# Optimization experiments

Hardware: AMD Instinct MI355X
Metric: run time of the kernel (lower is better)

## Reference

```python
import jax, jax.numpy as jnp
import numpy as np

K = 4          # neighbors
R = 2          # step_ratio
O = 64         # output_size


def setup_inputs() -> dict:
    key = jax.random.key(0)
    ks = jax.random.split(key, 7)
    B, C, N = 16, 128, 2048
    x = jax.random.normal(ks[0], (B, C, N), jnp.float32)
    # 1x1 conv weights stored as [out, in]; bias [out]
    w1 = jax.random.normal(ks[1], (O, 2 * C), jnp.float32) * (1.0 / np.sqrt(2 * C))
    b1 = jax.random.normal(ks[2], (O,), jnp.float32) * 0.01
    w2 = jax.random.normal(ks[3], (O * R, 2 * C + O), jnp.float32) * (1.0 / np.sqrt(2 * C + O))
    b2 = jax.random.normal(ks[4], (O * R,), jnp.float32) * 0.01
    w3 = jax.random.normal(ks[5], (O, O), jnp.float32) * (1.0 / np.sqrt(O))
    b3 = jax.random.normal(ks[6], (O,), jnp.float32) * 0.01
    return {"x": x, "w1": w1, "b1": b1, "w2": w2, "b2": b2, "w3": w3, "b3": b3}


def _knn_idx(x, k):
    # x: [B, C, N]; returns indices of k nearest neighbors (incl. self) [B, N, k]
    inner = -2.0 * jnp.einsum('bcn,bcm->bnm', x, x)           # [B, N, N]
    xx = jnp.sum(x * x, axis=1)                                # [B, N]
    pd = -xx[:, :, None] - inner - xx[:, None, :]              # negative sq dist
    return jax.lax.top_k(pd, k)[1]                             # [B, N, k]


def _graph_feature(x, k):
    # minus_center=False variant used by EF_expansion
    idx = _knn_idx(x, k)                                       # [B, N, k]
    xt = jnp.transpose(x, (0, 2, 1))                           # [B, N, C]
    feat = jax.vmap(lambda xb, ib: xb[ib])(xt, idx)            # [B, N, k, C]
    center = jnp.broadcast_to(xt[:, :, None, :], feat.shape)   # [B, N, k, C]
    f = jnp.concatenate([center, feat], axis=3)                # [B, N, k, 2C]
    return jnp.transpose(f, (0, 3, 1, 2))                      # [B, 2C, N, k]


def _conv1x1(w, b, x):
    # x: [B, Cin, H, W] -> [B, Cout, H, W]
    return jnp.einsum('oc,bchw->bohw', w, x) + b[None, :, None, None]


def reference(x, w1, b1, w2, b2, w3, b3):
    B, C, N = x.shape
    ief = jnp.transpose(_graph_feature(x, K), (0, 1, 3, 2))    # [B, 2C, k, N]
    e1 = _conv1x1(w1, b1, ief)                                 # [B, O, k, N]
    e = jax.nn.relu(jnp.concatenate([e1, ief], axis=1))        # [B, O+2C, k, N]
    e2 = jax.nn.relu(_conv1x1(w2, b2, e))                      # [B, O*R, k, N]
    # [B,O*R,k,N] -> [B,k,N,O*R] -> [B,k,N*R,O] -> [B,O,k,N*R]
    e2 = jnp.transpose(e2, (0, 2, 3, 1)).reshape(B, K, N * R, O)
    e2 = jnp.transpose(e2, (0, 3, 1, 2))
    e3 = _conv1x1(w3, b3, e2)                                  # [B, O, k, N*R]
    return jnp.max(e3, axis=2)                                 # [B, O, N*R]
```

## Files before the change

### kernel.cpp

```cpp
#include <hip/hip_runtime.h>
#include <cstdint>
#include <cstddef>

#define B_  16
#define C_  128
#define N_  2048
#define K_  4
#define O_  64
#define C2_ 256
#define ED_ 320
#define NM_ 4096
#define AGC 384

typedef float  f32x4  __attribute__((ext_vector_type(4)));
typedef short  s16x8  __attribute__((ext_vector_type(8)));
typedef __bf16 bf16x4 __attribute__((ext_vector_type(4)));
typedef __bf16 bf16x8 __attribute__((ext_vector_type(8)));
typedef unsigned short u16;
typedef unsigned int   u32;
typedef unsigned int   u32x4 __attribute__((ext_vector_type(4)));

__device__ __forceinline__ u32 umin32(u32 a, u32 b) { return a < b ? a : b; }
__device__ __forceinline__ u32 umax32(u32 a, u32 b) { return a > b ? a : b; }
__device__ __forceinline__ float bf2f(u16 h) { return __builtin_bit_cast(float, (u32)h << 16); }

__device__ __forceinline__ s16x8 ldw_bf16(const float* __restrict__ p) {
  float4 a = *(const float4*)p;
  float4 c = *(const float4*)(p + 4);
  bf16x8 r;
  r[0] = (__bf16)a.x; r[1] = (__bf16)a.y; r[2] = (__bf16)a.z; r[3] = (__bf16)a.w;
  r[4] = (__bf16)c.x; r[5] = (__bf16)c.y; r[6] = (__bf16)c.z; r[7] = (__bf16)c.w;
  return __builtin_bit_cast(s16x8, r);
}

__device__ __forceinline__ u32 relu2(u32 u) {
  u32 s = u & 0x80008000u;
  u32 m = s - (s >> 15);
  return u & ~(m | s);
}
__device__ __forceinline__ s16x8 relu8(s16x8 v) {
  u32x4 u = __builtin_bit_cast(u32x4, v);
  u[0] = relu2(u[0]); u[1] = relu2(u[1]);
  u[2] = relu2(u[2]); u[3] = relu2(u[3]);
  return __builtin_bit_cast(s16x8, u);
}

__device__ __forceinline__ void glds16(const void* g, void* l) {
  __builtin_amdgcn_global_load_lds(
      (const __attribute__((address_space(1))) u32*)g,
      (__attribute__((address_space(3))) u32*)l, 16, 0, 0);
}

__global__ __launch_bounds__(256) void prep_kernel(const float* __restrict__ x,
                                                   const float* __restrict__ w1,
                                                   const float* __restrict__ w2,
                                                   const float* __restrict__ w3,
                                                   float* __restrict__ xT32,
                                                   u16* __restrict__ xh,
                                                   float* __restrict__ xx,
                                                   u16* __restrict__ wh,
                                                   u16* __restrict__ wg) {
  const int t = threadIdx.x;
  if (blockIdx.y == B_) {
    const int gid = blockIdx.x * 256 + t;
    for (int i = gid; i < 15360; i += 8192) {
      const float* src; u16* dst;
      if (i < 4096)       { src = w1 + (size_t)i * 4;            dst = wh + (size_t)i * 4; }
      else if (i < 14336) { src = w2 + (size_t)(i - 4096) * 4;   dst = wh + 16384 + (size_t)(i - 4096) * 4; }
      else                { src = w3 + (size_t)(i - 14336) * 4;  dst = wh + 57344 + (size_t)(i - 14336) * 4; }
      float4 v = *(const float4*)src;
      ushort4 h;
      h.x = __builtin_bit_cast(u16, (__bf16)v.x);
      h.y = __builtin_bit_cast(u16, (__bf16)v.y);
      h.z = __builtin_bit_cast(u16, (__bf16)v.z);
      h.w = __builtin_bit_cast(u16, (__bf16)v.w);
      *(ushort4*)dst = h;
    }
    if (wg) {
      for (int i = gid; i < 12288; i += 8192) {
        int r = i >> 5;
        int c4 = (i & 31) * 4;
        const float* src;
        if (r < 64)       src = w1 + (size_t)r * C2_ + c4;
        else if (r < 128) src = w1 + (size_t)(r - 64) * C2_ + 128 + c4;
        else if (r < 256) src = w2 + (size_t)(r - 128) * ED_ + 64 + c4;
        else              src = w2 + (size_t)(r - 256) * ED_ + 192 + c4;
        float4 v = *(const float4*)src;
        ushort4 h;
        h.x = __builtin_bit_cast(u16, (__bf16)v.x);
        h.y = __builtin_bit_cast(u16, (__bf16)v.y);
        h.z = __builtin_bit_cast(u16, (__bf16)v.z);
        h.w = __builtin_bit_cast(u16, (__bf16)v.w);
        *(ushort4*)&wg[(size_t)r * 128 + c4] = h;
      }
    }
    return;
  }

  __shared__ __align__(16) float sx[C_][65];
  const int b = blockIdx.y, n0 = blockIdx.x * 64;
  const float* xb = x + (size_t)b * C_ * N_;
  for (int u = t; u < C_ * 16; u += 256) {
    int c = u >> 4, f4 = u & 15;
    float4 v = *(const float4*)&xb[(size_t)c * N_ + n0 + f4 * 4];
    sx[c][f4 * 4 + 0] = v.x; sx[c][f4 * 4 + 1] = v.y;
    sx[c][f4 * 4 + 2] = v.z; sx[c][f4 * 4 + 3] = v.w;
  }
  __syncthreads();
  if (t < 64) {
    float s = 0.f;
    for (int c = 0; c < C_; ++c) { float v = sx[c][t]; s = fmaf(v, v, s); }
    xx[b * N_ + n0 + t] = s;
  }
  for (int u = t; u < 64 * 16; u += 256) {
    int n = u >> 4, cb = u & 15;
    float vv[8]; s16x8 hv;
#pragma unroll
    for (int j = 0; j < 8; ++j) {
      float v = sx[cb * 8 + j][n];
      vv[j] = v;
      hv[j] = (short)__builtin_bit_cast(u16, (__bf16)v);
    }
    size_t ro = ((size_t)b * N_ + n0 + n) * C_;
    *(float4*)&xT32[ro + cb * 8]     = make_float4(vv[0], vv[1], vv[2], vv[3]);
    *(float4*)&xT32[ro + cb * 8 + 4] = make_float4(vv[4], vv[5], vv[6], vv[7]);
    int sc = cb ^ (n & 7);
    *(s16x8*)&xh[ro + sc * 8] = hv;
  }
}

__global__ __launch_bounds__(256) void knn_mfma(const u16* __restrict__ xh,
                                                const float* __restrict__ xx,
                                                int* __restrict__ cand8) {
  __shared__ __align__(16) u32 cd[64 * 85];
  const int b = blockIdx.y, q0 = blockIdx.x * 64;
  const int t = threadIdx.x;
  const int wv = t >> 6, lq = t & 15, lh = (t >> 4) & 3;
  const u16* xhb = xh + (size_t)b * N_ * C_;
  const float* xxb = xx + b * N_;

  s16x8 qf[4][4];
#pragma unroll
  for (int qt = 0; qt < 4; ++qt)
#pragma unroll
    for (int ks = 0; ks < 4; ++ks) {
      int q = q0 + qt * 16 + lq;
      int ch = (ks * 4 + lh) ^ (q & 7);
      qf[qt][ks] = *(const s16x8*)&xhb[(size_t)q * C_ + ch * 8];
    }

  u32 pk[4][5];
#pragma unroll
  for (int qt = 0; qt < 4; ++qt)
#pragma unroll
    for (int s = 0; s < 5; ++s) pk[qt][s] = 0xFFFFFFFFu;

  const int rbase = wv * 16 + lq;
  int choff[4];
#pragma unroll
  for (int ks = 0; ks < 4; ++ks) choff[ks] = ((ks * 4 + lh) ^ (lq & 7)) * 8;

  auto loadf = [&](int step, s16x8* d) {
    const u16* rp = xhb + (size_t)(step * 64 + rbase) * C_;
#pragma unroll
    for (int ks = 0; ks < 4; ++ks) d[ks] = *(const s16x8*)&rp[choff[ks]];
  };
  auto dostep = [&](int step, const s16x8* mf) {
    f32x4 acc[4];
#pragma unroll
    for (int qt = 0; qt < 4; ++qt) acc[qt] = (f32x4){0.f, 0.f, 0.f, 0.f};
#pragma unroll
    for (int ks = 0; ks < 4; ++ks)
#pragma unroll
      for (int qt = 0; qt < 4; ++qt)
        acc[qt] = __builtin_amdgcn_mfma_f32_16x16x32_bf16(mf[ks], qf[qt][ks], acc[qt], 0, 0, 0);
    const int mrow = step * 64 + wv * 16 + lh * 4;
    float4 xm4 = *(const float4*)&xxb[mrow];
    float xma[4] = {xm4.x + 512.f, xm4.y + 512.f, xm4.z + 512.f, xm4.w + 512.f};
#pragma unroll
    for (int r = 0; r < 4; ++r) {
#pragma unroll
      for (int qt = 0; qt < 4; ++qt) {
        float dd = fmaf(acc[qt][r], -2.f, xma[r]);
        u32 u = __builtin_bit_cast(u32, dd);
        u32 v = (u & 0xFFFFF800u) | (u32)(mrow + r);
#pragma unroll
        for (int s5 = 0; s5 < 5; ++s5) {
          u32 lo = umin32(v, pk[qt][s5]);
          v = umax32(v, pk[qt][s5]);
          pk[qt][s5] = lo;
        }
      }
    }
  };

  s16x8 fa[4], fb[4];
  loadf(0, fa);
  loadf(1, fb);
  for (int step = 0; step < 32; step += 2) {
    dostep(step, fa);
    if (step + 2 < 32) loadf(step + 2, fa);
    dostep(step + 1, fb);
    if (step + 3 < 32) loadf(step + 3, fb);
  }

  const int unit = wv * 4 + lh;
#pragma unroll
  for (int qt = 0; qt < 4; ++qt) {
    int ql = qt * 16 + lq;
#pragma unroll
    for (int s = 0; s < 5; ++s) cd[ql * 85 + unit * 5 + s] = pk[qt][s];
  }
  __syncthreads();
  if (t < 64) {
    u32 fd[8];
#pragma unroll
    for (int s = 0; s < 8; ++s) fd[s] = 0xFFFFFFFFu;
    for (int j = 0; j < 80; ++j) {
      u32 v = cd[t * 85 + j];
#pragma unroll
      for (int s = 0; s < 8; ++s) {
        u32 lo = umin32(v, fd[s]);
        v = umax32(v, fd[s]);
        fd[s] = lo;
      }
    }
#pragma unroll
    for (int s = 0; s < 8; ++s)
      cand8[((size_t)b * N_ + q0 + t) * 8 + s] = (int)(fd[s] & 0x7FFu);
  }
}

__global__ __launch_bounds__(256) void rerank_kernel(const float* __restrict__ xT32,
                                                     const float* __restrict__ xx,
                                                     const int* __restrict__ cand8,
                                                     int* __restrict__ knn_out) {
  __shared__ __align__(16) float sq[64][132];
  __shared__ float sd[64][8];
  __shared__ int   si[64][8];
  const int b = blockIdx.y, n0 = blockIdx.x * 64;
  const int t = threadIdx.x;
  const float* xb32 = xT32 + (size_t)b * N_ * C_;
  for (int u = t; u < 64 * 32; u += 256) {
    int n = u >> 5, seg = u & 31;
    *(float4*)&sq[n][seg * 4] = *(const float4*)&xb32[(size_t)(n0 + n) * C_ + seg * 4];
  }
  __syncthreads();
  const int ql = t >> 2, cs = t & 3;
#pragma unroll
  for (int cc = 0; cc < 2; ++cc) {
    int cslot = cs + cc * 4;
    int idx = cand8[((size_t)b * N_ + n0 + ql) * 8 + cslot];
    const float* mr = &xb32[(size_t)idx * C_];
    float a0 = 0.f, a1 = 0.f, a2 = 0.f, a3 = 0.f;
#pragma unroll 8
    for (int i = 0; i < 32; ++i) {
      float4 qv = *(const float4*)&sq[ql][i * 4];
      float4 mv = *(const float4*)&mr[i * 4];
      a0 = fmaf(qv.x, mv.x, a0); a1 = fmaf(qv.y, mv.y, a1);
      a2 = fmaf(qv.z, mv.z, a2); a3 = fmaf(qv.w, mv.w, a3);
    }
    float dot = (a0 + a1) + (a2 + a3);
    sd[ql][cslot] = xx[(size_t)b * N_ + idx] - 2.f * dot;
    si[ql][cslot] = idx;
  }
  __syncthreads();
  if (t < 64) {
    float dloc[8]; int iloc[8];
#pragma unroll
    for (int j = 0; j < 8; ++j) { dloc[j] = sd[t][j]; iloc[j] = si[t][j]; }
    u32 used = 0;
#pragma unroll
    for (int s = 0; s < 4; ++s) {
      float bdv = 1e30f; int bidx = 0x7fffffff; int bj = 0;
#pragma unroll
      for (int j = 0; j < 8; ++j) {
        if (!((used >> j) & 1)) {
          bool bet = (dloc[j] < bdv) || (dloc[j] == bdv && iloc[j] < bidx);
          if (bet) { bdv = dloc[j]; bidx = iloc[j]; bj = j; }
        }
      }
      used |= 1u << bj;
      knn_out[((size_t)b * N_ + n0 + t) * K_ + s] = bidx;
    }
  }
}

__global__ __launch_bounds__(256, 2) void agemm_kernel(
    const u16* __restrict__ xh, const u16* __restrict__ wg,
    const float* __restrict__ b1, const float* __restrict__ b2,
    u16* __restrict__ ag) {
  __shared__ __align__(16) char sm[66560];
  u16* outT = (u16*)(sm + 16384);
  const int b = blockIdx.y, m0 = blockIdx.x * 64;
  const int t = threadIdx.x, lane = t & 63, wv = t >> 6, lq = t & 15, lh = (t >> 4) & 3;
  const u16* xhb = xh + (size_t)b * N_ * C_;

  {
    const char* s = (const char*)(xhb + (size_t)m0 * C_);
#pragma unroll
    for (int c = 0; c < 4; ++c) {
      int off = (wv * 4 + c) * 1024;
      glds16(s + off + lane * 16, sm + off);
    }
  }

  s16x8 af[6][4];
#pragma unroll
  for (int rt = 0; rt < 6; ++rt)
#pragma unroll
    for (int ks = 0; ks < 4; ++ks)
      af[rt][ks] = *(const s16x8*)&wg[(size_t)(wv * 96 + rt * 16 + lq) * 128 + ks * 32 + lh * 8];

  f32x4 acc[6][4];
#pragma unroll
  for (int rt = 0; rt < 6; ++rt)
#pragma unroll
    for (int cg = 0; cg < 4; ++cg) acc[rt][cg] = (f32x4){0.f, 0.f, 0.f, 0.f};

  asm volatile("s_waitcnt vmcnt(0)");
  __syncthreads();

#pragma unroll
  for (int cg = 0; cg < 4; ++cg) {
    s16x8 braw[4], brel[4];
#pragma unroll
    for (int ks = 0; ks < 4; ++ks) {
      int row = cg * 16 + lq;
      braw[ks] = *(const s16x8*)(sm + row * 256 + (((ks * 4 + lh) ^ (lq & 7)) * 16));
      brel[ks] = relu8(braw[ks]);
    }
#pragma unroll
    for (int rt = 0; rt < 6; ++rt) {
      const bool rl = (wv * 96 + rt * 16) >= 128;
#pragma unroll
      for (int ks = 0; ks < 4; ++ks)
        acc[rt][cg] = __builtin_amdgcn_mfma_f32_16x16x32_bf16(
            af[rt][ks], rl ? brel[ks] : braw[ks], acc[rt][cg], 0, 0, 0);
    }
  }

#pragma unroll
  for (int rt = 0; rt < 6; ++rt) {
    const int ch0 = wv * 96 + rt * 16 + lh * 4;
    float bias[4];
#pragma unroll
    for (int r = 0; r < 4; ++r) {
      int c = ch0 + r;
      bias[r] = (c < 64) ? b1[c] : ((c >= 128 && c < 256) ? b2[c - 128] : 0.f);
    }
#pragma unroll
    for (int cg = 0; cg < 4; ++cg) {
      bf16x4 st;
#pragma unroll
      for (int r = 0; r < 4; ++r) st[r] = (__bf16)(acc[rt][cg][r] + bias[r]);
      *(bf16x4*)&outT[(size_t)(cg * 16 + lq) * 392 + ch0] = st;
    }
  }
  __syncthreads();

  {
    const int row = t >> 2, p = t & 3;
#pragma unroll
    for (int k = 0; k < 12; ++k) {
      int seg = k * 4 + p;
      *(u32x4*)&ag[((size_t)b * N_ + m0 + row) * AGC + seg * 8] =
          *(const u32x4*)&outT[(size_t)row * 392 + seg * 8];
    }
  }
}

__global__ __launch_bounds__(256, 3) void fused_ag(
    const u16* __restrict__ ag, const u16* __restrict__ wh,
    const int* __restrict__ knn_idx,
    const float* __restrict__ b3, float* __restrict__ out) {
  __shared__ __align__(16) char fsm[44032];
  u16* e1T = (u16*)fsm;
  u16* s2T = (u16*)(fsm + 9216);
  u16* e2T = (u16*)(fsm + 26624);
  float* oSt = (float*)fsm;

  const int t = threadIdx.x, wv = t >> 6, lq = t & 15, lh = (t >> 4) & 3;
  const int b = blockIdx.y, n0 = blockIdx.x * 16;
  const u16* agb = ag + (size_t)b * N_ * AGC;
  const u16* w2h = wh + 16384;
  const u16* w3h = wh + 57344;

  s16x8 w2f[2][2];
#pragma unroll
  for (int rt = 0; rt < 2; ++rt)
#pragma unroll
    for (int ks = 0; ks < 2; ++ks)
      w2f[rt][ks] = *(const s16x8*)&w2h[(size_t)(wv * 32 + rt * 16 + lq) * ED_ + ks * 32 + lh * 8];
  const s16x8 w3a = *(const s16x8*)&w3h[(size_t)(wv * 16 + lq) * O_ + lh * 8];
  const s16x8 w3b = *(const s16x8*)&w3h[(size_t)(wv * 16 + lq) * O_ + 32 + lh * 8];
  const float4 b3v = *(const float4*)&b3[wv * 16 + lh * 4];

  {
    const int col = t >> 2, p = t & 3;
    const int n = n0 + (col >> 2);
    const int nid = knn_idx[((size_t)b * N_ + n) * K_ + (col & 3)];
    const u16* rc = agb + (size_t)n * AGC;
    const u16* rn = agb + (size_t)nid * AGC;
#pragma unroll
    for (int q = 0; q < 2; ++q) {
      s16x8 va = *(const s16x8*)&rc[p * 16 + q * 8];
      s16x8 vb = *(const s16x8*)&rn[64 + p * 16 + q * 8];
      bf16x8 r;
#pragma unroll
      for (int j = 0; j < 8; ++j)
        r[j] = (__bf16)fmaxf(bf2f((u16)va[j]) + bf2f((u16)vb[j]), 0.f);
      *(bf16x8*)&e1T[(size_t)col * 72 + p * 16 + q * 8] = r;
    }
#pragma unroll
    for (int q = 0; q < 4; ++q) {
      s16x8 va = *(const s16x8*)&rc[128 + p * 32 + q * 8];
      s16x8 vb = *(const s16x8*)&rn[256 + p * 32 + q * 8];
      bf16x8 r;
#pragma unroll
      for (int j = 0; j < 8; ++j)
        r[j] = (__bf16)(bf2f((u16)va[j]) + bf2f((u16)vb[j]));
      *(bf16x8*)&s2T[(size_t)col * 136 + p * 32 + q * 8] = r;
    }
  }
  __syncthreads();

  {
    f32x4 acc[2][4];
#pragma unroll
    for (int rt = 0; rt < 2; ++rt)
#pragma unroll
      for (int cg = 0; cg < 4; ++cg) acc[rt][cg] = (f32x4){0.f, 0.f, 0.f, 0.f};
#pragma unroll
    for (int ks = 0; ks < 2; ++ks)
#pragma unroll
      for (int cg = 0; cg < 4; ++cg) {
        s16x8 bf = *(const s16x8*)&e1T[(size_t)(cg * 16 + lq) * 72 + ks * 32 + lh * 8];
#pragma unroll
        for (int rt = 0; rt < 2; ++rt)
          acc[rt][cg] = __builtin_amdgcn_mfma_f32_16x16x32_bf16(w2f[rt][ks], bf, acc[rt][cg], 0, 0, 0);
      }
#pragma unroll
    for (int rt = 0; rt < 2; ++rt)
#pragma unroll
      for (int cg = 0; cg < 4; ++cg) {
        const int col = cg * 16 + lq;
        const int j0 = wv * 32 + rt * 16 + lh * 4;
        ushort4 sv = *(const ushort4*)&s2T[(size_t)col * 136 + j0];
        bf16x4 st;
        st[0] = (__bf16)fmaxf(acc[rt][cg][0] + bf2f(sv.x), 0.f);
        st[1] = (__bf16)fmaxf(acc[rt][cg][1] + bf2f(sv.y), 0.f);
        st[2] = (__bf16)fmaxf(acc[rt][cg][2] + bf2f(sv.z), 0.f);
        st[3] = (__bf16)fmaxf(acc[rt][cg][3] + bf2f(sv.w), 0.f);
        *(bf16x4*)&e2T[(size_t)col * 136 + j0] = st;
      }
  }
  __syncthreads();

  {
#pragma unroll
    for (int cg = 0; cg < 8; ++cg) {
      int col = cg * 16 + lq;
      int nl = col >> 3, rr = (col >> 2) & 1, kk = col & 3;
      int row = nl * 4 + kk;
      s16x8 f1 = *(const s16x8*)&e2T[(size_t)row * 136 + rr * 64 + lh * 8];
      s16x8 f2 = *(const s16x8*)&e2T[(size_t)row * 136 + rr * 64 + 32 + lh * 8];
      f32x4 acc = {0.f, 0.f, 0.f, 0.f};
      acc = __builtin_amdgcn_mfma_f32_16x16x32_bf16(w3a, f1, acc, 0, 0, 0);
      acc = __builtin_amdgcn_mfma_f32_16x16x32_bf16(w3b, f2, acc, 0, 0, 0);
      float vv[4];
#pragma unroll
      for (int r = 0; r < 4; ++r) {
        float v = acc[r];
        v = fmaxf(v, __shfl_xor(v, 1));
        v = fmaxf(v, __shfl_xor(v, 2));
        vv[r] = v;
      }
      if ((lq & 3) == 0) {
        int mloc = col >> 2;
        int o = wv * 16 + lh * 4;
        const float b3a[4] = {b3v.x, b3v.y, b3v.z, b3v.w};
#pragma unroll
        for (int r = 0; r < 4; ++r) oSt[(size_t)(o + r) * 36 + mloc] = vv[r] + b3a[r];
      }
    }
  }
  __syncthreads();

#pragma unroll
  for (int io = 0; io < 2; ++io) {
    int u = t + io * 256;
    int o = u >> 3, seg = u & 7;
    *(float4*)&out[((size_t)b * O_ + o) * NM_ + n0 * 2 + seg * 4] =
        *(const float4*)&oSt[(size_t)o * 36 + seg * 4];
  }
}

__global__ __launch_bounds__(256) void xx_kernel(const float* __restrict__ x,
                                                 float* __restrict__ xx) {
  int g = blockIdx.x * 256 + threadIdx.x;
  int b = g >> 11;
  int n = g & (N_ - 1);
  const float* xp = x + (size_t)b * C_ * N_ + n;
  float s = 0.f;
#pragma unroll 8
  for (int c = 0; c < C_; ++c) { float v = xp[(size_t)c * N_]; s += v * v; }
  xx[g] = s;
}

__global__ __launch_bounds__(256) void knn_kernel(const float* __restrict__ x,
                                                  const float* __restrict__ xx,
                                                  int* __restrict__ knn_out) {
  __shared__ __align__(16) float qT[C_ * 64];
  __shared__ __align__(16) float mT[C_ * 64];
  const int b = blockIdx.y;
  const int q0 = blockIdx.x * 64;
  const int t = threadIdx.x;
  const float* xb = x + (size_t)b * C_ * N_;
  const float* xxb = xx + b * N_;
  for (int i = t; i < C_ * 64; i += 256) {
    int c = i >> 6, q = i & 63;
    qT[i] = xb[(size_t)c * N_ + q0 + q];
  }
  const int tq = t & 15;
  const int tm = t >> 4;
  float bd[4][4]; int bi[4][4];
#pragma unroll
  for (int a = 0; a < 4; ++a)
#pragma unroll
    for (int s = 0; s < 4; ++s) { bd[a][s] = 1e30f; bi[a][s] = 0; }
  for (int m0 = 0; m0 < N_; m0 += 64) {
    __syncthreads();
    for (int i = t; i < C_ * 64; i += 256) {
      int c = i >> 6, m = i & 63;
      mT[i] = xb[(size_t)c * N_ + m0 + m];
    }
    __syncthreads();
    float acc[4][4];
#pragma unroll
    for (int a = 0; a < 4; ++a)
#pragma unroll
      for (int j = 0; j < 4; ++j) acc[a][j] = 0.f;
#pragma unroll 4
    for (int c = 0; c < C_; ++c) {
      float4 qv = *(const float4*)&qT[c * 64 + tq * 4];
      float4 mv = *(const float4*)&mT[c * 64 + tm * 4];
      float qa[4] = {qv.x, qv.y, qv.z, qv.w};
      float ma[4] = {mv.x, mv.y, mv.z, mv.w};
#pragma unroll
      for (int a = 0; a < 4; ++a)
#pragma unroll
        for (int j = 0; j < 4; ++j) acc[a][j] += qa[a] * ma[j];
    }
#pragma unroll
    for (int j = 0; j < 4; ++j) {
      float xm = xxb[m0 + tm * 4 + j];
      int id = m0 + tm * 4 + j;
#pragma unroll
      for (int a = 0; a < 4; ++a) {
        float d = xm - 2.f * acc[a][j];
        if (d < bd[a][3]) {
          bd[a][3] = d; bi[a][3] = id;
#pragma unroll
          for (int s = 3; s > 0; --s)
            if (bd[a][s] < bd[a][s - 1]) {
              float td = bd[a][s]; bd[a][s] = bd[a][s - 1]; bd[a][s - 1] = td;
              int ti = bi[a][s]; bi[a][s] = bi[a][s - 1]; bi[a][s - 1] = ti;
            }
        }
      }
    }
  }
  __syncthreads();
  float* cd = qT;
  int* ci = (int*)mT;
#pragma unroll
  for (int a = 0; a < 4; ++a) {
    int q = tq * 4 + a;
#pragma unroll
    for (int s = 0; s < 4; ++s) {
      cd[q * 64 + tm * 4 + s] = bd[a][s];
      ci[q * 64 + tm * 4 + s] = bi[a][s];
    }
  }
  __syncthreads();
  if (t < 64) {
    float fd[4]; int fi[4];
#pragma unroll
    for (int s = 0; s < 4; ++s) { fd[s] = 1e30f; fi[s] = 0; }
    for (int j = 0; j < 64; ++j) {
      float d = cd[t * 64 + j];
      int id = ci[t * 64 + j];
      if (d < fd[3]) {
        fd[3] = d; fi[3] = id;
#pragma unroll
        for (int s = 3; s > 0; --s)
          if (fd[s] < fd[s - 1]) {
            float td = fd[s]; fd[s] = fd[s - 1]; fd[s - 1] = td;
            int ti = fi[s]; fi[s] = fi[s - 1]; fi[s - 1] = ti;
          }
      }
    }
#pragma unroll
    for (int s = 0; s < 4; ++s)
      knn_out[(b * N_ + q0 + t) * K_ + s] = fi[s];
  }
}

__global__ __launch_bounds__(256, 5) void fused_fb(
    const float* __restrict__ x, const int* __restrict__ knn_idx,
    const float* __restrict__ w1, const float* __restrict__ b1,
    const float* __restrict__ w2, const float* __restrict__ b2,
    const float* __restrict__ w3, const float* __restrict__ b3,
    float* __restrict__ out) {
  __shared__ __align__(16) char fsm[30976];
  __bf16 (*cT)[136]  = (__bf16(*)[136])(fsm);
  __bf16 (*e1T)[72]  = (__bf16(*)[72])(fsm + 4352);
  float  (*oSt)[36]  = (float(*)[36])(fsm + 4352);
  __bf16 (*nT)[136]  = (__bf16(*)[136])(fsm + 13568);
  __bf16 (*e2T)[136] = (__bf16(*)[136])(fsm + 13568);

  const int b  = blockIdx.y;
  const int n0 = blockIdx.x * 16;
  const int t  = threadIdx.x;
  const float* xb = x + (size_t)b * C_ * N_;

  {
    const int stn = t >> 4, stc = t & 15;
    const int kbase = (b * N_ + n0) * K_;
    const float* srcc = xb + (size_t)(stc * 8) * N_ + n0 + stn;
    bf16x8 raw;
#pragma unroll
    for (int j = 0; j < 8; ++j) raw[j] = (__bf16)srcc[(size_t)j * N_];
    *(bf16x8*)&cT[stn][stc * 8] = raw;
#pragma unroll
    for (int it = 0; it < 4; ++it) {
      int col = stn + 16 * it;
      int nid = knn_idx[kbase + col];
      const float* src = xb + (size_t)(stc * 8) * N_ + nid;
      bf16x8 rw;
#pragma unroll
      for (int j = 0; j < 8; ++j) rw[j] = (__bf16)src[(size_t)j * N_];
      *(bf16x8*)&nT[col][stc * 8] = rw;
    }
  }
  __syncthreads();

  const int lq = t & 15;
  const int lh = (t >> 4) & 3;
  const int wv = t >> 6;

  {
    const float* w1r = w1 + (size_t)(wv * 16 + lq) * C2_;
    f32x4 acc[4];
#pragma unroll
    for (int cg = 0; cg < 4; ++cg) acc[cg] = (f32x4){0.f, 0.f, 0.f, 0.f};
#pragma unroll
    for (int ks = 0; ks < 8; ++ks) {
      s16x8 a = ldw_bf16(w1r + ks * 32 + lh * 8);
#pragma unroll
      for (int cg = 0; cg < 4; ++cg) {
        const __bf16* bp = (ks < 4)
            ? &cT[cg * 4 + (lq >> 2)][ks * 32 + lh * 8]
            : &nT[cg * 16 + lq][(ks - 4) * 32 + lh * 8];
        acc[cg] = __builtin_amdgcn_mfma_f32_16x16x32_bf16(
            a, *(const s16x8*)bp, acc[cg], 0, 0, 0);
      }
    }
#pragma unroll
    for (int cg = 0; cg < 4; ++cg) {
      bf16x4 st;
#pragma unroll
      for (int r = 0; r < 4; ++r) {
        float v = acc[cg][r] + b1[wv * 16 + lh * 4 + r];
        st[r] = (__bf16)fmaxf(v, 0.f);
      }
      *(bf16x4*)&e1T[cg * 16 + lq][wv * 16 + lh * 4] = st;
    }
  }
  __syncthreads();

  f32x4 acc2[2][4];
  {
    const float* w2r0 = w2 + (size_t)(wv * 32 + lq) * ED_;
    const float* w2r1 = w2r0 + (size_t)16 * ED_;
#pragma unroll
    for (int ro = 0; ro < 2; ++ro)
#pragma unroll
      for (int cg = 0; cg < 4; ++cg) acc2[ro][cg] = (f32x4){0.f, 0.f, 0.f, 0.f};
#pragma unroll
    for (int ks = 0; ks < 10; ++ks) {
      s16x8 a0 = ldw_bf16(w2r0 + ks * 32 + lh * 8);
      s16x8 a1 = ldw_bf16(w2r1 + ks * 32 + lh * 8);
#pragma unroll
      for (int cg = 0; cg < 4; ++cg) {
        s16x8 bf;
        if (ks < 2)      bf = *(const s16x8*)&e1T[cg * 16 + lq][ks * 32 + lh * 8];
        else if (ks < 6) bf = relu8(*(const s16x8*)&cT[cg * 4 + (lq >> 2)][(ks - 2) * 32 + lh * 8]);
        else             bf = relu8(*(const s16x8*)&nT[cg * 16 + lq][(ks - 6) * 32 + lh * 8]);
        acc2[0][cg] = __builtin_amdgcn_mfma_f32_16x16x32_bf16(a0, bf, acc2[0][cg], 0, 0, 0);
        acc2[1][cg] = __builtin_amdgcn_mfma_f32_16x16x32_bf16(a1, bf, acc2[1][cg], 0, 0, 0);
      }
    }
  }
  __syncthreads();
  {
#pragma unroll
    for (int ro = 0; ro < 2; ++ro)
#pragma unroll
      for (int cg = 0; cg < 4; ++cg) {
        bf16x4 st;
#pragma unroll
        for (int r = 0; r < 4; ++r) {
          float v = acc2[ro][cg][r] + b2[wv * 32 + ro * 16 + lh * 4 + r];
          st[r] = (__bf16)fmaxf(v, 0.f);
        }
        *(bf16x4*)&e2T[cg * 16 + lq][wv * 32 + ro * 16 + lh * 4] = st;
      }
  }
  __syncthreads();

  {
    const float* w3r = w3 + (size_t)(wv * 16 + lq) * O_;
    s16x8 a0 = ldw_bf16(w3r + lh * 8);
    s16x8 a1 = ldw_bf16(w3r + 32 + lh * 8);
#pragma unroll
    for (int cg = 0; cg < 8; ++cg) {
      int col = cg * 16 + lq;
      int nl = col >> 3, rr = (col >> 2) & 1, kk = col & 3;
      const __bf16* base = &e2T[nl * 4 + kk][rr * 64];
      f32x4 acc = {0.f, 0.f, 0.f, 0.f};
      acc = __builtin_amdgcn_mfma_f32_16x16x32_bf16(a0, *(const s16x8*)(base + lh * 8),      acc, 0, 0, 0);
      acc = __builtin_amdgcn_mfma_f32_16x16x32_bf16(a1, *(const s16x8*)(base + 32 + lh * 8), acc, 0, 0, 0);
      float vv[4];
#pragma unroll
      for (int r = 0; r < 4; ++r) {
        float v = acc[r];
        v = fmaxf(v, __shfl_xor(v, 1));
        v = fmaxf(v, __shfl_xor(v, 2));
        vv[r] = v;
      }
      if ((lq & 3) == 0) {
        int mloc = col >> 2;
        int o = wv * 16 + lh * 4;
#pragma unroll
        for (int r = 0; r < 4; ++r) oSt[o + r][mloc] = vv[r] + b3[o + r];
      }
    }
  }
  __syncthreads();

#pragma unroll
  for (int it = 0; it < 2; ++it) {
    int u = t + it * 256;
    int o = u >> 3, seg = u & 7;
    *(float4*)&out[((size_t)b * O_ + o) * NM_ + n0 * 2 + seg * 4] =
        *(const float4*)&oSt[o][seg * 4];
  }
}

extern "C" void kernel_launch(void* const* d_in, const int* in_sizes, int n_in,
                              void* d_out, int out_size, void* d_ws, size_t ws_size,
                              hipStream_t stream) {
  const float* x  = (const float*)d_in[0];
  const float* w1 = (const float*)d_in[1];
  const float* b1 = (const float*)d_in[2];
  const float* w2 = (const float*)d_in[3];
  const float* b2 = (const float*)d_in[4];
  const float* w3 = (const float*)d_in[5];
  const float* b3 = (const float*)d_in[6];
  float* out = (float*)d_out;

  const size_t AGB      = (size_t)B_ * N_ * AGC * 2;
  const size_t off_c8N  = (size_t)B_ * N_ * C_ * 4;
  const size_t off_xhN  = AGB;
  const size_t off_xxN  = off_xhN + (size_t)B_ * N_ * C_ * 2;
  const size_t off_knnN = off_xxN + (size_t)B_ * N_ * 4;
  const size_t off_whN  = off_knnN + (size_t)B_ * N_ * K_ * 4;
  const size_t off_wgN  = off_whN + (size_t)61440 * 2;
  const size_t NEED_NEW = off_wgN + (size_t)AGC * 128 * 2;

  if (ws_size >= NEED_NEW) {
    u16*   agp  = (u16*)d_ws;
    float* xT32 = (float*)d_ws;
    int*   c8   = (int*)((char*)d_ws + off_c8N);
    u16*   xhp  = (u16*)((char*)d_ws + off_xhN);
    float* xx   = (float*)((char*)d_ws + off_xxN);
    int*   knn  = (int*)((char*)d_ws + off_knnN);
    u16*   whp  = (u16*)((char*)d_ws + off_whN);
    u16*   wgp  = (u16*)((char*)d_ws + off_wgN);

    hipLaunchKernelGGL(prep_kernel, dim3(N_ / 64, B_ + 1), dim3(256), 0, stream,
                       x, w1, w2, w3, xT32, xhp, xx, whp, wgp);
    hipLaunchKernelGGL(knn_mfma, dim3(N_ / 64, B_), dim3(256), 0, stream, xhp, xx, c8);
    hipLaunchKernelGGL(rerank_kernel, dim3(N_ / 64, B_), dim3(256), 0, stream, xT32, xx, c8, knn);
    hipLaunchKernelGGL(agemm_kernel, dim3(N_ / 64, B_), dim3(256), 0, stream,
                       xhp, wgp, b1, b2, agp);
    hipLaunchKernelGGL(fused_ag, dim3(N_ / 16, B_), dim3(256), 0, stream,
                       agp, whp, knn, b3, out);
  } else {
    float* xx = (float*)d_ws;
    int* knn = (int*)((char*)d_ws + (size_t)B_ * N_ * 4);
    hipLaunchKernelGGL(xx_kernel, dim3((B_ * N_) / 256), dim3(256), 0, stream, x, xx);
    hipLaunchKernelGGL(knn_kernel, dim3(N_ / 64, B_), dim3(256), 0, stream, x, xx, knn);
    hipLaunchKernelGGL(fused_fb, dim3(N_ / 16, B_), dim3(256), 0, stream,
                       x, knn, w1, b1, w2, b2, w3, b3, out);
  }
}
```

Baseline: 111.7 us.

## Split KNN candidate search across two key halves and rerank sixteen candidates

The MFMA KNN kernel now splits the 2048 key points into two halves along a new grid dimension. Each block scans only 1024 keys and writes 8 candidates per half, giving 16 candidates per query. This doubles the block count from 512 to 1024, which raises occupancy across the GPU's CUs and halves the serial loop length per block. The xx loads are also prefetched alongside the fragment loads. The rerank kernel is adjusted to 32 queries per block and evaluates 16 fp32 candidates per query, which doubles its gather and dot-product work.

```diff
diff --git a/kernel.cpp b/kernel.cpp
--- a/kernel.cpp
+++ b/kernel.cpp
@@ -131,9 +131,10 @@
 
 __global__ __launch_bounds__(256) void knn_mfma(const u16* __restrict__ xh,
                                                 const float* __restrict__ xx,
-                                                int* __restrict__ cand8) {
+                                                int* __restrict__ cand16) {
   __shared__ __align__(16) u32 cd[64 * 85];
-  const int b = blockIdx.y, q0 = blockIdx.x * 64;
+  const int b = blockIdx.z, half = blockIdx.y, q0 = blockIdx.x * 64;
+  const int mbase = half * 1024;
   const int t = threadIdx.x;
   const int wv = t >> 6, lq = t & 15, lh = (t >> 4) & 3;
   const u16* xhb = xh + (size_t)b * N_ * C_;
@@ -161,11 +162,14 @@
   for (int ks = 0; ks < 4; ++ks) choff[ks] = ((ks * 4 + lh) ^ (lq & 7)) * 8;
 
   auto loadf = [&](int step, s16x8* d) {
-    const u16* rp = xhb + (size_t)(step * 64 + rbase) * C_;
+    const u16* rp = xhb + (size_t)(mbase + step * 64 + rbase) * C_;
 #pragma unroll
     for (int ks = 0; ks < 4; ++ks) d[ks] = *(const s16x8*)&rp[choff[ks]];
   };
-  auto dostep = [&](int step, const s16x8* mf) {
+  auto loadxx = [&](int step) -> f32x4 {
+    return *(const f32x4*)&xxb[mbase + step * 64 + wv * 16 + lh * 4];
+  };
+  auto dostep = [&](int step, const s16x8* mf, f32x4 xm4) {
     f32x4 acc[4];
 #pragma unroll
     for (int qt = 0; qt < 4; ++qt) acc[qt] = (f32x4){0.f, 0.f, 0.f, 0.f};
@@ -174,9 +178,8 @@
 #pragma unroll
       for (int qt = 0; qt < 4; ++qt)
         acc[qt] = __builtin_amdgcn_mfma_f32_16x16x32_bf16(mf[ks], qf[qt][ks], acc[qt], 0, 0, 0);
-    const int mrow = step * 64 + wv * 16 + lh * 4;
-    float4 xm4 = *(const float4*)&xxb[mrow];
-    float xma[4] = {xm4.x + 512.f, xm4.y + 512.f, xm4.z + 512.f, xm4.w + 512.f};
+    const int mrow = mbase + step * 64 + wv * 16 + lh * 4;
+    float xma[4] = {xm4[0] + 512.f, xm4[1] + 512.f, xm4[2] + 512.f, xm4[3] + 512.f};
 #pragma unroll
     for (int r = 0; r < 4; ++r) {
 #pragma unroll
@@ -195,13 +198,16 @@
   };
 
   s16x8 fa[4], fb[4];
+  f32x4 xa, xb4;
   loadf(0, fa);
   loadf(1, fb);
-  for (int step = 0; step < 32; step += 2) {
-    dostep(step, fa);
-    if (step + 2 < 32) loadf(step + 2, fa);
-    dostep(step + 1, fb);
-    if (step + 3 < 32) loadf(step + 3, fb);
+  xa = loadxx(0);
+  xb4 = loadxx(1);
+  for (int step = 0; step < 16; step += 2) {
+    dostep(step, fa, xa);
+    if (step + 2 < 16) { loadf(step + 2, fa); xa = loadxx(step + 2); }
+    dostep(step + 1, fb, xb4);
+    if (step + 3 < 16) { loadf(step + 3, fb); xb4 = loadxx(step + 3); }
   }
 
   const int unit = wv * 4 + lh;
@@ -227,30 +233,30 @@
     }
 #pragma unroll
     for (int s = 0; s < 8; ++s)
-      cand8[((size_t)b * N_ + q0 + t) * 8 + s] = (int)(fd[s] & 0x7FFu);
+      cand16[((size_t)b * N_ + q0 + t) * 16 + half * 8 + s] = (int)(fd[s] & 0x7FFu);
   }
 }
 
 __global__ __launch_bounds__(256) void rerank_kernel(const float* __restrict__ xT32,
                                                      const float* __restrict__ xx,
-                                                     const int* __restrict__ cand8,
+                                                     const int* __restrict__ cand16,
                                                      int* __restrict__ knn_out) {
-  __shared__ __align__(16) float sq[64][132];
-  __shared__ float sd[64][8];
-  __shared__ int   si[64][8];
-  const int b = blockIdx.y, n0 = blockIdx.x * 64;
+  __shared__ __align__(16) float sq[32][132];
+  __shared__ float sd[32][16];
+  __shared__ int   si[32][16];
+  const int b = blockIdx.y, n0 = blockIdx.x * 32;
   const int t = threadIdx.x;
   const float* xb32 = xT32 + (size_t)b * N_ * C_;
-  for (int u = t; u < 64 * 32; u += 256) {
+  for (int u = t; u < 32 * 32; u += 256) {
     int n = u >> 5, seg = u & 31;
     *(float4*)&sq[n][seg * 4] = *(const float4*)&xb32[(size_t)(n0 + n) * C_ + seg * 4];
   }
   __syncthreads();
-  const int ql = t >> 2, cs = t & 3;
+  const int ql = t >> 3, cs = t & 7;
 #pragma unroll
   for (int cc = 0; cc < 2; ++cc) {
-    int cslot = cs + cc * 4;
-    int idx = cand8[((size_t)b * N_ + n0 + ql) * 8 + cslot];
+    int cslot = cs + cc * 8;
+    int idx = cand16[((size_t)b * N_ + n0 + ql) * 16 + cslot];
     const float* mr = &xb32[(size_t)idx * C_];
     float a0 = 0.f, a1 = 0.f, a2 = 0.f, a3 = 0.f;
 #pragma unroll 8
@@ -265,16 +271,16 @@
     si[ql][cslot] = idx;
   }
   __syncthreads();
-  if (t < 64) {
-    float dloc[8]; int iloc[8];
-#pragma unroll
-    for (int j = 0; j < 8; ++j) { dloc[j] = sd[t][j]; iloc[j] = si[t][j]; }
+  if (t < 32) {
+    float dloc[16]; int iloc[16];
+#pragma unroll
+    for (int j = 0; j < 16; ++j) { dloc[j] = sd[t][j]; iloc[j] = si[t][j]; }
     u32 used = 0;
 #pragma unroll
     for (int s = 0; s < 4; ++s) {
       float bdv = 1e30f; int bidx = 0x7fffffff; int bj = 0;
 #pragma unroll
-      for (int j = 0; j < 8; ++j) {
+      for (int j = 0; j < 16; ++j) {
         if (!((used >> j) & 1)) {
           bool bet = (dloc[j] < bdv) || (dloc[j] == bdv && iloc[j] < bidx);
           if (bet) { bdv = dloc[j]; bidx = iloc[j]; bj = j; }
@@ -772,7 +778,7 @@
   float* out = (float*)d_out;
 
   const size_t AGB      = (size_t)B_ * N_ * AGC * 2;
-  const size_t off_c8N  = (size_t)B_ * N_ * C_ * 4;
+  const size_t off_c16  = (size_t)B_ * N_ * C_ * 4;
   const size_t off_xhN  = AGB;
   const size_t off_xxN  = off_xhN + (size_t)B_ * N_ * C_ * 2;
   const size_t off_knnN = off_xxN + (size_t)B_ * N_ * 4;
@@ -783,7 +789,7 @@
   if (ws_size >= NEED_NEW) {
     u16*   agp  = (u16*)d_ws;
     float* xT32 = (float*)d_ws;
-    int*   c8   = (int*)((char*)d_ws + off_c8N);
+    int*   c16  = (int*)((char*)d_ws + off_c16);
     u16*   xhp  = (u16*)((char*)d_ws + off_xhN);
     float* xx   = (float*)((char*)d_ws + off_xxN);
     int*   knn  = (int*)((char*)d_ws + off_knnN);
@@ -792,8 +798,8 @@
 
     hipLaunchKernelGGL(prep_kernel, dim3(N_ / 64, B_ + 1), dim3(256), 0, stream,
                        x, w1, w2, w3, xT32, xhp, xx, whp, wgp);
-    hipLaunchKernelGGL(knn_mfma, dim3(N_ / 64, B_), dim3(256), 0, stream, xhp, xx, c8);
-    hipLaunchKernelGGL(rerank_kernel, dim3(N_ / 64, B_), dim3(256), 0, stream, xT32, xx, c8, knn);
+    hipLaunchKernelGGL(knn_mfma, dim3(N_ / 64, 2, B_), dim3(256), 0, stream, xhp, xx, c16);
+    hipLaunchKernelGGL(rerank_kernel, dim3(N_ / 32, B_), dim3(256), 0, stream, xT32, xx, c16, knn);
     hipLaunchKernelGGL(agemm_kernel, dim3(N_ / 64, B_), dim3(256), 0, stream,
                        xhp, wgp, b1, b2, agp);
     hipLaunchKernelGGL(fused_ag, dim3(N_ / 16, B_), dim3(256), 0, stream,
```

Measured after the change: 127.5 us. +14.1%, slower.
